# Kernel tuning notes

Measured on AMD Instinct MI355X. Metric: run time of the kernel, lower is better.

## Reference

```python
import jax, jax.numpy as jnp
import numpy as np

EPS = 1e-5
GROUPS = 8
OUT_PLANES = 256
GP = OUT_PLANES // GROUPS  # group_planes = 32


def _bn_eval(x, p, ch_axis):
    # p: [4, C] = (gamma, beta, running_mean, running_var); eval-mode batchnorm
    shape = [1] * x.ndim
    shape[ch_axis] = -1
    g, b, m, v = (p[i].reshape(shape) for i in range(4))
    return g * (x - m) * jax.lax.rsqrt(v + EPS) + b


def _make_bn(key, ch):
    k1, k2, k3, k4 = jax.random.split(key, 4)
    gamma = jax.random.uniform(k1, (ch,)) + 0.5
    beta = jax.random.normal(k2, (ch,)) * 0.1
    mean = jax.random.normal(k3, (ch,)) * 0.1
    var = jax.random.uniform(k4, (ch,)) + 0.5
    return jnp.stack([gamma, beta, mean, var])  # [4, ch]


def setup_inputs() -> dict:
    key = jax.random.key(0)
    ks = jax.random.split(key, 6)
    N, C, D, Hh, Ww = 1, 256, 16, 32, 64
    x = jax.random.normal(ks[0], (N, C, D, Hh, Ww), dtype=jnp.float32)
    # qkv 1x1 conv weight: [out_planes*2, in_planes]
    qkv_w = jax.random.normal(ks[1], (OUT_PLANES * 2, C), dtype=jnp.float32) * np.sqrt(1.0 / C)
    # relative positional table: [group_planes*2, 2*H-1]
    relative = jax.random.normal(ks[2], (GP * 2, 2 * Ww - 1), dtype=jnp.float32) * np.sqrt(1.0 / GP)
    bn_qkv = _make_bn(ks[3], OUT_PLANES * 2)
    bn_sim = _make_bn(ks[4], GROUPS * 3)
    bn_out = _make_bn(ks[5], OUT_PLANES * 2)
    return {"x": x, "qkv_w": qkv_w, "relative": relative,
            "bn_qkv": bn_qkv, "bn_sim": bn_sim, "bn_out": bn_out}


def reference(x, qkv_w, relative, bn_qkv, bn_sim, bn_out):
    N, C, D, Hh, Ww = x.shape
    G, OP, gp = GROUPS, OUT_PLANES, GP
    # width == 0: permute(0,2,3,1,4) -> [N, D, Hh, C, Ww]; attend along Ww
    xp = jnp.transpose(x, (0, 2, 3, 1, 4))
    H = Ww
    B = N * D * Hh
    xr = xp.reshape(B, C, H)
    # 1x1 conv + BN over channels
    qkv = jnp.einsum('oc,bch->boh', qkv_w, xr)
    qkv = _bn_eval(qkv, bn_qkv, 1)
    qkv = qkv.reshape(B, G, 2 * gp, H)
    q = qkv[:, :, : gp // 2]          # [B,G,gp/2,H]
    k = qkv[:, :, gp // 2: gp]        # [B,G,gp/2,H]
    v = qkv[:, :, gp:]                # [B,G,gp,H]
    # relative-position gather: emb[c,i,j] = relative[c, i-j+H-1]
    idx = jnp.arange(H)[:, None] - jnp.arange(H)[None, :] + H - 1  # [H,H]
    emb = relative[:, idx]            # [2*gp, H, H]
    q_e = emb[: gp // 2]
    k_e = emb[gp // 2: gp]
    v_e = emb[gp:]
    qr = jnp.einsum('bgci,cij->bgij', q, q_e)
    kr = jnp.einsum('bgci,cij->bgji', k, k_e)  # einsum + transpose(2,3) fused
    qk = jnp.einsum('bgci,bgcj->bgij', q, k)
    sim = jnp.concatenate([qk, qr, kr], axis=1)  # [B, 3G, H, H]
    sim = _bn_eval(sim, bn_sim, 1)
    sim = sim.reshape(B, 3, G, H, H).sum(axis=1)
    sim = jax.nn.softmax(sim, axis=3)
    sv = jnp.einsum('bgij,bgcj->bgci', sim, v)
    sve = jnp.einsum('bgij,cij->bgci', sim, v_e)
    so = jnp.concatenate([sv, sve], axis=-1).reshape(B, 2 * OP, H)
    out = _bn_eval(so, bn_out, 1)
    out = out.reshape(N, D, Hh, OP, 2, H).sum(axis=-2)
    out = jnp.transpose(out, (0, 3, 1, 2, 4))  # [N, OP, D, Hh, Ww]
    return out
```

## Files before the change

kernel.cpp:

```cpp
#include <hip/hip_runtime.h>

#define EPS 1e-5f

typedef _Float16 half4_t __attribute__((ext_vector_type(4)));
typedef _Float16 half8_t __attribute__((ext_vector_type(8)));
typedef float floatx4 __attribute__((ext_vector_type(4)));

__device__ __forceinline__ unsigned short f2hb(float f) {
  _Float16 h = (_Float16)f;
  return __builtin_bit_cast(unsigned short, h);
}
__device__ __forceinline__ float hb2f(unsigned short u) {
  return (float)__builtin_bit_cast(_Float16, u);
}
__device__ __forceinline__ unsigned int pack2(float a, float b) {
  return (unsigned int)f2hb(a) | ((unsigned int)f2hb(b) << 16);
}

#define WS_QKT 16777216
#define WS_WH 33554432
#define WS_RELTQ 33816576
#define WS_RELTK 33820672
#define WS_RELV 33824768
#define WS_BNSF 33832960
#define WS_BNOSC 33833088
#define WS_BNOSH 33835136
#define WS_BNQSC 33837184
#define WS_BNQSH 33839232

__global__ __launch_bounds__(256) void k_prep(const float* __restrict__ W,
                                              const float* __restrict__ bnq,
                                              const float* __restrict__ rel,
                                              const float* __restrict__ bns,
                                              const float* __restrict__ bno,
                                              char* __restrict__ ws) {
  const int bid = blockIdx.x, tid = threadIdx.x;
  if (bid < 8) {
    unsigned short* Wh = (unsigned short*)(ws + WS_WH);
    const int base = bid * 16384;
#pragma unroll
    for (int u = 0; u < 16; ++u) {
      const int i = base + u * 1024 + tid * 4;
      const float4 v = *reinterpret_cast<const float4*>(&W[i]);
      uint2 p;
      p.x = pack2(v.x, v.y);
      p.y = pack2(v.z, v.w);
      *reinterpret_cast<uint2*>(&Wh[i]) = p;
    }
  } else {
    unsigned short* relTq = (unsigned short*)(ws + WS_RELTQ);
    unsigned short* relTk = (unsigned short*)(ws + WS_RELTK);
    unsigned short* relV = (unsigned short*)(ws + WS_RELV);
    float* bnsF = (float*)(ws + WS_BNSF);
    float* bnoSc = (float*)(ws + WS_BNOSC);
    float* bnoSh = (float*)(ws + WS_BNOSH);
    float* bnqSc = (float*)(ws + WS_BNQSC);
    float* bnqSh = (float*)(ws + WS_BNQSH);
    for (int idx = tid; idx < 2048; idx += 256) {
      const int t = idx >> 4, c = idx & 15;
      relTq[idx] = (t < 127) ? f2hb(rel[c * 127 + t]) : (unsigned short)0;
      relTk[idx] = (t < 127) ? f2hb(rel[(16 + c) * 127 + t]) : (unsigned short)0;
    }
    for (int idx = tid; idx < 4096; idx += 256) {
      const int c = idx >> 7, t = idx & 127;
      relV[idx] = (t < 127) ? f2hb(rel[(32 + c) * 127 + t]) : (unsigned short)0;
    }
    if (tid < 8) {
      const int g = tid;
      const float scA = bns[g] / sqrtf(bns[72 + g] + EPS);
      const float scB = bns[8 + g] / sqrtf(bns[72 + 8 + g] + EPS);
      const float scC = bns[16 + g] / sqrtf(bns[72 + 16 + g] + EPS);
      const float shv = (bns[24 + g] - bns[48 + g] * scA) +
                        (bns[24 + 8 + g] - bns[48 + 8 + g] * scB) +
                        (bns[24 + 16 + g] - bns[48 + 16 + g] * scC);
      bnsF[g * 4 + 0] = scA;
      bnsF[g * 4 + 1] = scB;
      bnsF[g * 4 + 2] = scC;
      bnsF[g * 4 + 3] = shv;
    }
    for (int idx = tid; idx < 512; idx += 256) {
      const float sc = bno[idx] / sqrtf(bno[1536 + idx] + EPS);
      bnoSc[idx] = sc;
      bnoSh[idx] = bno[512 + idx] - bno[1024 + idx] * sc;
      const float qc = bnq[idx] / sqrtf(bnq[1536 + idx] + EPS);
      bnqSc[idx] = qc;
      bnqSh[idx] = bnq[512 + idx] - bnq[1024 + idx] * qc;
    }
  }
}

__global__ __launch_bounds__(512, 4) void k_qkv(const float* __restrict__ x,
                                                char* __restrict__ ws) {
  const unsigned short* Wh = (const unsigned short*)(ws + WS_WH);
  const float* bnqSc = (const float*)(ws + WS_BNQSC);
  const float* bnqSh = (const float*)(ws + WS_BNQSH);
  unsigned short* qkv_h = (unsigned short*)ws;
  unsigned short* qkT = (unsigned short*)(ws + WS_QKT);
  __shared__ __align__(16) char arena[36864];
  unsigned short* xT = (unsigned short*)arena;
  unsigned short* qk_t = (unsigned short*)arena;

  const int tid = threadIdx.x;
  const int lane = tid & 63;
  const int w = tid >> 6;
  const int l15 = lane & 15, kg = lane >> 4;
  const size_t b = blockIdx.x;
  const int n0g = (int)b * 64;

  {
    const int k = tid >> 1;
    const int nb = (tid & 1) * 32;
    const float* src = x + (size_t)k * 32768 + n0g + nb;
    unsigned short hv[32];
#pragma unroll
    for (int u = 0; u < 8; ++u) {
      const float4 v4 = *reinterpret_cast<const float4*>(src + u * 4);
      hv[u * 4 + 0] = f2hb(v4.x);
      hv[u * 4 + 1] = f2hb(v4.y);
      hv[u * 4 + 2] = f2hb(v4.z);
      hv[u * 4 + 3] = f2hb(v4.w);
    }
#pragma unroll
    for (int e = 0; e < 32; ++e) xT[(nb + e) * 280 + k] = hv[e];
  }
  __syncthreads();

  floatx4 acc[4][4] = {};
#pragma unroll
  for (int kk = 0; kk < 8; ++kk) {
    half8_t af[4], bf[4];
#pragma unroll
    for (int fm = 0; fm < 4; ++fm)
      af[fm] = *reinterpret_cast<const half8_t*>(Wh + (size_t)(w * 64 + fm * 16 + l15) * 256 +
                                                 kk * 32 + kg * 8);
#pragma unroll
    for (int fn = 0; fn < 4; ++fn)
      bf[fn] = *reinterpret_cast<const half8_t*>(xT + (fn * 16 + l15) * 280 + kk * 32 + kg * 8);
#pragma unroll
    for (int fm = 0; fm < 4; ++fm)
#pragma unroll
      for (int fn = 0; fn < 4; ++fn)
        acc[fm][fn] = __builtin_amdgcn_mfma_f32_16x16x32_f16(af[fm], bf[fn], acc[fm][fn], 0, 0, 0);
  }
  __syncthreads();

  const int o0 = w * 64;
#pragma unroll
  for (int fm = 0; fm < 4; ++fm) {
    const float4 sc4 = *reinterpret_cast<const float4*>(&bnqSc[o0 + fm * 16 + kg * 4]);
    const float4 sh4 = *reinterpret_cast<const float4*>(&bnqSh[o0 + fm * 16 + kg * 4]);
#pragma unroll
    for (int fn = 0; fn < 4; ++fn) {
      const int h = fn * 16 + l15;
      const float v0 = fmaf(acc[fm][fn][0], sc4.x, sh4.x);
      const float v1 = fmaf(acc[fm][fn][1], sc4.y, sh4.y);
      const float v2 = fmaf(acc[fm][fn][2], sc4.z, sh4.z);
      const float v3 = fmaf(acc[fm][fn][3], sc4.w, sh4.w);
      if (fm < 2) {
        uint2 p;
        p.x = pack2(v0, v1);
        p.y = pack2(v2, v3);
        *reinterpret_cast<uint2*>(&qk_t[w * 2304 + h * 36 + fm * 16 + kg * 4]) = p;
      } else {
        const int cb = (fm - 2) * 16 + kg * 4;
        unsigned short* dst = &qkv_h[((b * 8 + w) * 32 + cb) * 64 + h];
        dst[0] = f2hb(v0);
        dst[64] = f2hb(v1);
        dst[128] = f2hb(v2);
        dst[192] = f2hb(v3);
      }
    }
  }
  __syncthreads();
#pragma unroll
  for (int it = 0; it < 4; ++it) {
    const int idx = it * 512 + tid;
    const int g2 = idx >> 8, e = idx & 255;
    const int h = e >> 2, c0 = (e & 3) * 8;
    const unsigned short* srcp = &qk_t[g2 * 2304 + h * 36 + c0];
    const uint2 a = *reinterpret_cast<const uint2*>(srcp);
    const uint2 b2 = *reinterpret_cast<const uint2*>(srcp + 4);
    uint4 wv;
    wv.x = a.x;
    wv.y = a.y;
    wv.z = b2.x;
    wv.w = b2.y;
    *reinterpret_cast<uint4*>(&qkT[((b * 8 + g2) * 64 + h) * 32 + c0]) = wv;
  }
}

#define QKS 36
#define MTS 68
#define PBS 72
#define PPS 136

__global__ __launch_bounds__(256, 4) void k_attn(const char* __restrict__ ws,
                                                 float* __restrict__ out) {
  const unsigned short* qkv_h = (const unsigned short*)ws;
  const unsigned short* qkTg = (const unsigned short*)(ws + WS_QKT);
  const unsigned short* relTq = (const unsigned short*)(ws + WS_RELTQ);
  const unsigned short* relTk = (const unsigned short*)(ws + WS_RELTK);
  const unsigned short* relV = (const unsigned short*)(ws + WS_RELV);
  const float* bnsF = (const float*)(ws + WS_BNSF);
  const float* bnoSc = (const float*)(ws + WS_BNOSC);
  const float* bnoSh = (const float*)(ws + WS_BNOSH);

  __shared__ __align__(16) char arena[39424];
  unsigned short* qkL = (unsigned short*)arena;
  unsigned short* M1T = (unsigned short*)(arena + 4608);
  unsigned short* M2T = (unsigned short*)(arena + 22016);
  unsigned short* Pb = (unsigned short*)arena;
  unsigned short* Pp = (unsigned short*)(arena + 9216);
  unsigned short* Vb = (unsigned short*)(arena + 26624);
  float* rowsumL = (float*)(arena + 31232);

  const int tid = threadIdx.x;
  const int lane = tid & 63;
  const int wid = tid >> 6;
  const int l15 = lane & 15, kg = lane >> 4;
  const int bg = blockIdx.x;
  const int b = bg >> 3, g = bg & 7;

  {
    const uint4 qv =
        *reinterpret_cast<const uint4*>(&qkTg[(size_t)(((b << 3) + g)) * 2048 + tid * 8]);
    const int i = tid >> 2, c0 = (tid & 3) * 8;
    uint2 lo, hi;
    lo.x = qv.x;
    lo.y = qv.y;
    hi.x = qv.z;
    hi.y = qv.w;
    *reinterpret_cast<uint2*>(&qkL[i * QKS + c0]) = lo;
    *reinterpret_cast<uint2*>(&qkL[i * QKS + c0 + 4]) = hi;
  }
  __syncthreads();

  floatx4 qkreg[4];
  {
    half4_t brq[8], brk[8];
#pragma unroll
    for (int nt = 0; nt < 8; ++nt) {
      brq[nt] = *reinterpret_cast<const half4_t*>(&relTq[(nt * 16 + l15) * 16 + kg * 4]);
      brk[nt] = *reinterpret_cast<const half4_t*>(&relTk[(nt * 16 + l15) * 16 + kg * 4]);
    }
    const half4_t aq = *reinterpret_cast<const half4_t*>(&qkL[(wid * 16 + l15) * QKS + kg * 4]);
    const half4_t ak =
        *reinterpret_cast<const half4_t*>(&qkL[(wid * 16 + l15) * QKS + 16 + kg * 4]);
#pragma unroll
    for (int nt = 0; nt < 4; ++nt) {
      const half4_t bq =
          *reinterpret_cast<const half4_t*>(&qkL[(nt * 16 + l15) * QKS + 16 + kg * 4]);
      const floatx4 z = {};
      qkreg[nt] = __builtin_amdgcn_mfma_f32_16x16x16f16(aq, bq, z, 0, 0, 0);
    }
    const int mcol = wid * 16 + kg * 4;
#pragma unroll
    for (int nt = 0; nt < 8; ++nt) {
      const floatx4 z = {};
      const floatx4 cr = __builtin_amdgcn_mfma_f32_16x16x16f16(aq, brq[nt], z, 0, 0, 0);
      uint2 p;
      p.x = pack2(cr[0], cr[1]);
      p.y = pack2(cr[2], cr[3]);
      *reinterpret_cast<uint2*>(&M1T[(nt * 16 + l15) * MTS + mcol]) = p;
    }
#pragma unroll
    for (int nt = 0; nt < 8; ++nt) {
      const floatx4 z = {};
      const floatx4 cr = __builtin_amdgcn_mfma_f32_16x16x16f16(ak, brk[nt], z, 0, 0, 0);
      uint2 p;
      p.x = pack2(cr[0], cr[1]);
      p.y = pack2(cr[2], cr[3]);
      *reinterpret_cast<uint2*>(&M2T[(nt * 16 + l15) * MTS + mcol]) = p;
    }
  }
  __syncthreads();

  const uint4 vld = *reinterpret_cast<const uint4*>(
      &qkv_h[(((size_t)b * 8 + g) * 32 + (tid >> 3)) * 64 + (tid & 7) * 8]);
  float sreg[4][4];
  {
    const float4 bf = *reinterpret_cast<const float4*>(&bnsF[g * 4]);
#pragma unroll
    for (int nt = 0; nt < 4; ++nt) {
      const int j = nt * 16 + l15;
#pragma unroll
      for (int r = 0; r < 4; ++r) {
        const int i = wid * 16 + kg * 4 + r;
        const int d = i - j + 63;
        const float qr = hb2f(M1T[d * MTS + i]);
        const float kr = hb2f(M2T[(126 - d) * MTS + j]);
        sreg[nt][r] = fmaf(bf.x, qkreg[nt][r], fmaf(bf.y, qr, fmaf(bf.z, kr, bf.w)));
      }
    }
  }
  __syncthreads();

  float sm[4];
#pragma unroll
  for (int r = 0; r < 4; ++r) {
    float m = fmaxf(fmaxf(sreg[0][r], sreg[1][r]), fmaxf(sreg[2][r], sreg[3][r]));
    m = fmaxf(m, __shfl_xor(m, 1));
    m = fmaxf(m, __shfl_xor(m, 2));
    m = fmaxf(m, __shfl_xor(m, 4));
    m = fmaxf(m, __shfl_xor(m, 8));
    float s = 0.f;
#pragma unroll
    for (int nt = 0; nt < 4; ++nt) {
      sreg[nt][r] = __expf(sreg[nt][r] - m);
      s += sreg[nt][r];
    }
    s += __shfl_xor(s, 1);
    s += __shfl_xor(s, 2);
    s += __shfl_xor(s, 4);
    s += __shfl_xor(s, 8);
    sm[r] = s;
  }
#pragma unroll
  for (int r = 0; r < 4; ++r) {
    const int i = wid * 16 + kg * 4 + r;
    const int z0 = l15 * 4;
    if (z0 + 3 < i) {
      uint2 zz;
      zz.x = 0u;
      zz.y = 0u;
      *reinterpret_cast<uint2*>(&Pp[i * PPS + z0]) = zz;
    } else if (z0 >= i) {
      uint2 zz;
      zz.x = 0u;
      zz.y = 0u;
      *reinterpret_cast<uint2*>(&Pp[i * PPS + z0 + 64]) = zz;
    } else {
#pragma unroll
      for (int e = 0; e < 4; ++e) {
        const int z = z0 + e;
        Pp[i * PPS + (z < i ? z : z + 64)] = 0;
      }
    }
#pragma unroll
    for (int nt = 0; nt < 4; ++nt) {
      const int j = nt * 16 + l15;
      const unsigned short pv = f2hb(sreg[nt][r]);
      Pb[i * PBS + j] = pv;
      Pp[i * PPS + i + 63 - j] = pv;
    }
    if (l15 == 0) rowsumL[i] = sm[r];
  }
  {
    *reinterpret_cast<uint4*>(&Vb[(tid >> 3) * PBS + (tid & 7) * 8]) = vld;
  }
  __syncthreads();

  floatx4 sva[2] = {}, svea[2] = {};
#pragma unroll
  for (int kk = 0; kk < 2; ++kk) {
    const half8_t pbf =
        *reinterpret_cast<const half8_t*>(&Pb[(wid * 16 + l15) * PBS + kk * 32 + kg * 8]);
#pragma unroll
    for (int cf = 0; cf < 2; ++cf) {
      const half8_t vb =
          *reinterpret_cast<const half8_t*>(&Vb[(cf * 16 + l15) * PBS + kk * 32 + kg * 8]);
      sva[cf] = __builtin_amdgcn_mfma_f32_16x16x32_f16(vb, pbf, sva[cf], 0, 0, 0);
    }
  }
#pragma unroll
  for (int kk = 0; kk < 4; ++kk) {
    const half8_t ppf =
        *reinterpret_cast<const half8_t*>(&Pp[(wid * 16 + l15) * PPS + kk * 32 + kg * 8]);
#pragma unroll
    for (int cf = 0; cf < 2; ++cf) {
      const half8_t rb =
          *reinterpret_cast<const half8_t*>(&relV[(cf * 16 + l15) * 128 + kk * 32 + kg * 8]);
      svea[cf] = __builtin_amdgcn_mfma_f32_16x16x32_f16(rb, ppf, svea[cf], 0, 0, 0);
    }
  }
  {
    const int i = wid * 16 + l15;
    const float inv = 1.0f / rowsumL[i];
#pragma unroll
    for (int cf = 0; cf < 2; ++cf) {
#pragma unroll
      for (int reg = 0; reg < 4; ++reg) {
        const int c = cf * 16 + kg * 4 + reg;
        const int ch = ((g << 5) + c) * 2;
        const float2 scv = *reinterpret_cast<const float2*>(&bnoSc[ch]);
        const float2 shv = *reinterpret_cast<const float2*>(&bnoSh[ch]);
        out[(size_t)((g << 5) + c) * 32768 + (size_t)b * 64 + i] =
            fmaf(scv.x, sva[cf][reg] * inv, shv.x) + fmaf(scv.y, svea[cf][reg] * inv, shv.y);
      }
    }
  }
}

extern "C" void kernel_launch(void* const* d_in, const int* in_sizes, int n_in,
                              void* d_out, int out_size, void* d_ws, size_t ws_size,
                              hipStream_t stream) {
  const float* x = (const float*)d_in[0];
  const float* qkv_w = (const float*)d_in[1];
  const float* relative = (const float*)d_in[2];
  const float* bn_qkv = (const float*)d_in[3];
  const float* bn_sim = (const float*)d_in[4];
  const float* bn_out = (const float*)d_in[5];
  float* out = (float*)d_out;
  char* ws = (char*)d_ws;

  k_prep<<<9, 256, 0, stream>>>(qkv_w, bn_qkv, relative, bn_sim, bn_out, ws);
  k_qkv<<<512, 512, 0, stream>>>(x, ws);
  k_attn<<<4096, 256, 0, stream>>>(ws, out);
}
```

Measured before the change: 80.79 us.

## Scatter relative-position products directly into skewed sim layout, shrink LDS, add setprio

The qr/kr MFMA results are now pre-scaled by the BN factors and scattered straight into 64x64 row-major buffers indexed by (i,j), replacing the 128-row transposed staging arrays. The sim assembly then reads both terms with a simple row-major access instead of diagonal gathers. LDS per block shrinks, which may allow more resident blocks. s_setprio is also raised around the MFMA sections. In exchange, the scatter uses scalar 16-bit stores with bounds checks, which could cause bank conflicts and extra instructions.

Measured after the change: 84.28 us. 4.3% more time.

```diff
diff --git a/kernel.cpp b/kernel.cpp
--- a/kernel.cpp
+++ b/kernel.cpp
@@ -190,7 +190,7 @@
 }
 
 #define QKS 36
-#define MTS 68
+#define SBS 66
 #define PBS 72
 #define PPS 136
 
@@ -205,10 +205,10 @@
   const float* bnoSc = (const float*)(ws + WS_BNOSC);
   const float* bnoSh = (const float*)(ws + WS_BNOSH);
 
-  __shared__ __align__(16) char arena[39424];
+  __shared__ __align__(16) char arena[31488];
   unsigned short* qkL = (unsigned short*)arena;
-  unsigned short* M1T = (unsigned short*)(arena + 4608);
-  unsigned short* M2T = (unsigned short*)(arena + 22016);
+  unsigned short* Sb1 = (unsigned short*)(arena + 4608);
+  unsigned short* Sb2 = (unsigned short*)(arena + 13056);
   unsigned short* Pb = (unsigned short*)arena;
   unsigned short* Pp = (unsigned short*)(arena + 9216);
   unsigned short* Vb = (unsigned short*)(arena + 26624);
@@ -220,6 +220,7 @@
   const int l15 = lane & 15, kg = lane >> 4;
   const int bg = blockIdx.x;
   const int b = bg >> 3, g = bg & 7;
+  const float4 bf = *reinterpret_cast<const float4*>(&bnsF[g * 4]);
 
   {
     const uint4 qv =
@@ -237,15 +238,16 @@
 
   floatx4 qkreg[4];
   {
+    const half4_t aq = *reinterpret_cast<const half4_t*>(&qkL[(wid * 16 + l15) * QKS + kg * 4]);
+    const half4_t ak =
+        *reinterpret_cast<const half4_t*>(&qkL[(wid * 16 + l15) * QKS + 16 + kg * 4]);
     half4_t brq[8], brk[8];
 #pragma unroll
     for (int nt = 0; nt < 8; ++nt) {
       brq[nt] = *reinterpret_cast<const half4_t*>(&relTq[(nt * 16 + l15) * 16 + kg * 4]);
       brk[nt] = *reinterpret_cast<const half4_t*>(&relTk[(nt * 16 + l15) * 16 + kg * 4]);
     }
-    const half4_t aq = *reinterpret_cast<const half4_t*>(&qkL[(wid * 16 + l15) * QKS + kg * 4]);
-    const half4_t ak =
-        *reinterpret_cast<const half4_t*>(&qkL[(wid * 16 + l15) * QKS + 16 + kg * 4]);
+    __builtin_amdgcn_s_setprio(1);
 #pragma unroll
     for (int nt = 0; nt < 4; ++nt) {
       const half4_t bq =
@@ -258,39 +260,42 @@
     for (int nt = 0; nt < 8; ++nt) {
       const floatx4 z = {};
       const floatx4 cr = __builtin_amdgcn_mfma_f32_16x16x16f16(aq, brq[nt], z, 0, 0, 0);
-      uint2 p;
-      p.x = pack2(cr[0], cr[1]);
-      p.y = pack2(cr[2], cr[3]);
-      *reinterpret_cast<uint2*>(&M1T[(nt * 16 + l15) * MTS + mcol]) = p;
+      const int t = nt * 16 + l15;
+#pragma unroll
+      for (int reg = 0; reg < 4; ++reg) {
+        const int i = mcol + reg;
+        const int j = i - t + 63;
+        if (j >= 0 && j < 64) Sb1[i * SBS + j] = f2hb(bf.y * cr[reg]);
+      }
     }
 #pragma unroll
     for (int nt = 0; nt < 8; ++nt) {
       const floatx4 z = {};
       const floatx4 cr = __builtin_amdgcn_mfma_f32_16x16x16f16(ak, brk[nt], z, 0, 0, 0);
-      uint2 p;
-      p.x = pack2(cr[0], cr[1]);
-      p.y = pack2(cr[2], cr[3]);
-      *reinterpret_cast<uint2*>(&M2T[(nt * 16 + l15) * MTS + mcol]) = p;
-    }
+      const int t = nt * 16 + l15;
+#pragma unroll
+      for (int reg = 0; reg < 4; ++reg) {
+        const int jj = mcol + reg;
+        const int i = jj - t + 63;
+        if (i >= 0 && i < 64) Sb2[i * SBS + jj] = f2hb(bf.z * cr[reg]);
+      }
+    }
+    __builtin_amdgcn_s_setprio(0);
   }
   __syncthreads();
 
   const uint4 vld = *reinterpret_cast<const uint4*>(
       &qkv_h[(((size_t)b * 8 + g) * 32 + (tid >> 3)) * 64 + (tid & 7) * 8]);
   float sreg[4][4];
-  {
-    const float4 bf = *reinterpret_cast<const float4*>(&bnsF[g * 4]);
-#pragma unroll
-    for (int nt = 0; nt < 4; ++nt) {
-      const int j = nt * 16 + l15;
-#pragma unroll
-      for (int r = 0; r < 4; ++r) {
-        const int i = wid * 16 + kg * 4 + r;
-        const int d = i - j + 63;
-        const float qr = hb2f(M1T[d * MTS + i]);
-        const float kr = hb2f(M2T[(126 - d) * MTS + j]);
-        sreg[nt][r] = fmaf(bf.x, qkreg[nt][r], fmaf(bf.y, qr, fmaf(bf.z, kr, bf.w)));
-      }
+#pragma unroll
+  for (int nt = 0; nt < 4; ++nt) {
+    const int j = nt * 16 + l15;
+#pragma unroll
+    for (int r = 0; r < 4; ++r) {
+      const int i = wid * 16 + kg * 4 + r;
+      const float qr = hb2f(Sb1[i * SBS + j]);
+      const float kr = hb2f(Sb2[i * SBS + j]);
+      sreg[nt][r] = fmaf(bf.x, qkreg[nt][r], qr + kr + bf.w);
     }
   }
   __syncthreads();
@@ -351,6 +356,7 @@
   __syncthreads();
 
   floatx4 sva[2] = {}, svea[2] = {};
+  __builtin_amdgcn_s_setprio(1);
 #pragma unroll
   for (int kk = 0; kk < 2; ++kk) {
     const half8_t pbf =
@@ -373,6 +379,7 @@
       svea[cf] = __builtin_amdgcn_mfma_f32_16x16x32_f16(rb, ppf, svea[cf], 0, 0, 0);
     }
   }
+  __builtin_amdgcn_s_setprio(0);
   {
     const int i = wid * 16 + l15;
     const float inv = 1.0f / rowsumL[i];
```
